# Kernel optimization log

Hardware: AMD Instinct MI355X
Metric: run time of the kernel (lower is better)

## Reference

```python
import jax, jax.numpy as jnp
from jax import lax
import numpy as np

B, C, H, W = 64, 1, 512, 512
N_MULT = 1  # len(mul_approx_func_arr)


def setup_inputs() -> dict:
    key = jax.random.key(0)
    k1, = jax.random.split(key, 1)
    # image-like pixel inputs in [0, 255)
    inp = jax.random.uniform(k1, (B, C, H, W), dtype=jnp.float32) * 255.0
    # Gaussian kernel params, tiled per multiplier variant (as in __init__)
    base = jnp.array([1.0, 2.0, 1.0, 2.0, 4.0, 2.0, 1.0, 2.0, 1.0], dtype=jnp.float32) / 16.0
    weight = jnp.tile(base[None, :], (N_MULT, 1))            # [N_MULT, 9]
    weight_factor = jnp.full((N_MULT, 1), 16.0, jnp.float32)  # [N_MULT, 1]
    return {"input": inp, "weight": weight, "weight_factor": weight_factor}


def _ste_quantize(x):
    # QuantizeGrad: forward = clamp(round(x), 0.001, inf); backward = identity (STE)
    q = jnp.clip(jnp.round(x), 0.001, None)
    return x + lax.stop_gradient(q - x)


def reference(input, weight, weight_factor):
    # in-place .data clamp (no grad through the clamp itself)
    wc_data = weight + lax.stop_gradient(jnp.clip(weight, 0.001, 0.999) - weight)
    wf_data = weight_factor + lax.stop_gradient(jnp.clip(weight_factor, 1.001, 254.999) - weight_factor)
    # hardtanh clamps (identity in-range after the data clamp)
    wc = jnp.clip(wc_data, 0.0, 1.0)
    wf = jnp.clip(wf_data, 1.0, 255.0)
    outs = []
    for ii in range(N_MULT):
        # weight_rounded: 9-element 3x3 kernel via STE quantization
        wr = _ste_quantize(wc[ii] * wf[ii])          # [9]
        kernel = wr.reshape(1, 1, 3, 3)
        # accurate_mult_only summed over the 9 taps == 3x3 conv, padding=1.
        # The approximate-multiplier forward value (mul_wrapper, emulated here as
        # exact multiply, index=1 accurate) is written into x.data, so forward
        # value and gradient path coincide under this emulation.
        y = lax.conv_general_dilated(
            input, kernel.astype(input.dtype),
            window_strides=(1, 1), padding=((1, 1), (1, 1)),
            dimension_numbers=("NCHW", "OIHW", "NCHW"))
        outs.append(y)
    # torch.stack(output, 0): [N_MULT, B, C, H, W]
    return jnp.stack(outs, 0)
```

## Files before the change

kernel.cpp:

```cpp
#include <hip/hip_runtime.h>


#define BB 64
#define HH 512
#define WW 512
#define W4 (WW / 4)
#define RR 4

__global__ __launch_bounds__(256) void gauss3x3_kernel(
    const float* __restrict__ in,
    const float* __restrict__ wgt,
    const float* __restrict__ wfac,
    float* __restrict__ out)
{
    float wf = fminf(fmaxf(wfac[0], 1.001f), 254.999f);
    float k[9];
#pragma unroll
    for (int i = 0; i < 9; ++i) {
        float wc = fminf(fmaxf(wgt[i], 0.001f), 0.999f);
        k[i] = fmaxf(rintf(wc * wf), 0.001f);
    }

    int tid   = blockIdx.x * blockDim.x + threadIdx.x;
    int x4    = tid & (W4 - 1);
    int strip = (tid >> 7) & (HH / RR - 1);
    int b     = tid >> 14;
    if (b >= BB) return;

    const int y0 = strip * RR;
    const int x0 = x4 * 4;
    const float* img  = in  + (size_t)b * HH * WW;
    float*       outp = out + (size_t)b * HH * WW;

    float4 acc[RR];
#pragma unroll
    for (int i = 0; i < RR; ++i) acc[i] = make_float4(0.f, 0.f, 0.f, 0.f);

#pragma unroll
    for (int j = 0; j < RR + 2; ++j) {
        const int ry = y0 - 1 + j;
        float4 c = make_float4(0.f, 0.f, 0.f, 0.f);
        float  l = 0.f, r = 0.f;
        if (ry >= 0 && ry < HH) {
            const float* row = img + (size_t)ry * WW;
            c = *(const float4*)(row + x0);
            l = (x0 > 0)      ? row[x0 - 1] : 0.f;
            r = (x0 + 4 < WW) ? row[x0 + 4] : 0.f;
        }
#pragma unroll
        for (int t = 0; t < 3; ++t) {
            const int i = j - t;
            if (i >= 0 && i < RR) {
                const float kl = k[t * 3 + 0];
                const float kc = k[t * 3 + 1];
                const float kr = k[t * 3 + 2];
                acc[i].x = fmaf(kl, l,   fmaf(kc, c.x, fmaf(kr, c.y, acc[i].x)));
                acc[i].y = fmaf(kl, c.x, fmaf(kc, c.y, fmaf(kr, c.z, acc[i].y)));
                acc[i].z = fmaf(kl, c.y, fmaf(kc, c.z, fmaf(kr, c.w, acc[i].z)));
                acc[i].w = fmaf(kl, c.z, fmaf(kc, c.w, fmaf(kr, r,   acc[i].w)));
            }
        }
    }

#pragma unroll
    for (int i = 0; i < RR; ++i)
        *(float4*)(outp + (size_t)(y0 + i) * WW + x0) = acc[i];
}

extern "C" void kernel_launch(void* const* d_in, const int* in_sizes, int n_in,
                              void* d_out, int out_size, void* d_ws, size_t ws_size,
                              hipStream_t stream) {
    const float* in   = (const float*)d_in[0];
    const float* wgt  = (const float*)d_in[1];
    const float* wfac = (const float*)d_in[2];
    float* out = (float*)d_out;

    const int total = BB * (HH / RR) * W4;
    const int block = 256;
    const int grid  = total / block;
    gauss3x3_kernel<<<grid, block, 0, stream>>>(in, wgt, wfac, out);
}
```

Baseline: 119.3 us.

## Map one wavefront per row strip and share halos via lane shuffles

Each 64-lane wavefront now covers a full 512-wide row strip, with every lane handling two float4 columns. Left and right halo pixels come from neighbouring lanes through shuffles instead of extra scalar global loads. Outputs are written with nontemporal stores to avoid cache pollution. The grid halves, so each thread does more work and holds more registers, and the shuffles add cross-lane instructions.

```diff
diff --git a/kernel.cpp b/kernel.cpp
--- a/kernel.cpp
+++ b/kernel.cpp
@@ -4,8 +4,9 @@
 #define BB 64
 #define HH 512
 #define WW 512
-#define W4 (WW / 4)
 #define RR 4
+
+typedef float vfloat4 __attribute__((ext_vector_type(4)));
 
 __global__ __launch_bounds__(256) void gauss3x3_kernel(
     const float* __restrict__ in,
@@ -21,31 +22,44 @@
         k[i] = fmaxf(rintf(wc * wf), 0.001f);
     }
 
-    int tid   = blockIdx.x * blockDim.x + threadIdx.x;
-    int x4    = tid & (W4 - 1);
-    int strip = (tid >> 7) & (HH / RR - 1);
-    int b     = tid >> 14;
+    const int gtid  = blockIdx.x * blockDim.x + threadIdx.x;
+    const int lane  = threadIdx.x & 63;
+    const int wid   = gtid >> 6;
+    const int strip = wid & (HH / RR - 1);
+    const int b     = wid >> 7;
     if (b >= BB) return;
 
     const int y0 = strip * RR;
-    const int x0 = x4 * 4;
     const float* img  = in  + (size_t)b * HH * WW;
     float*       outp = out + (size_t)b * HH * WW;
 
-    float4 acc[RR];
+    float4 acc1[RR], acc2[RR];
 #pragma unroll
-    for (int i = 0; i < RR; ++i) acc[i] = make_float4(0.f, 0.f, 0.f, 0.f);
+    for (int i = 0; i < RR; ++i) {
+        acc1[i] = make_float4(0.f, 0.f, 0.f, 0.f);
+        acc2[i] = make_float4(0.f, 0.f, 0.f, 0.f);
+    }
 
 #pragma unroll
     for (int j = 0; j < RR + 2; ++j) {
         const int ry = y0 - 1 + j;
-        float4 c = make_float4(0.f, 0.f, 0.f, 0.f);
-        float  l = 0.f, r = 0.f;
+        float4 c1 = make_float4(0.f, 0.f, 0.f, 0.f);
+        float4 c2 = c1;
+        float l1 = 0.f, r1 = 0.f, l2 = 0.f, r2 = 0.f;
         if (ry >= 0 && ry < HH) {
-            const float* row = img + (size_t)ry * WW;
-            c = *(const float4*)(row + x0);
-            l = (x0 > 0)      ? row[x0 - 1] : 0.f;
-            r = (x0 + 4 < WW) ? row[x0 + 4] : 0.f;
+            const float4* row4 = (const float4*)(img + (size_t)ry * WW);
+            c1 = row4[lane];
+            c2 = row4[lane + 64];
+            float l1n = __shfl_up(c1.w, 1);
+            float r1n = __shfl_down(c1.x, 1);
+            float l2n = __shfl_up(c2.w, 1);
+            float r2n = __shfl_down(c2.x, 1);
+            float b0  = __shfl(c2.x, 0);
+            float a63 = __shfl(c1.w, 63);
+            l1 = (lane == 0)  ? 0.f : l1n;
+            r1 = (lane == 63) ? b0  : r1n;
+            l2 = (lane == 0)  ? a63 : l2n;
+            r2 = (lane == 63) ? 0.f : r2n;
         }
 #pragma unroll
         for (int t = 0; t < 3; ++t) {
@@ -54,17 +68,26 @@
                 const float kl = k[t * 3 + 0];
                 const float kc = k[t * 3 + 1];
                 const float kr = k[t * 3 + 2];
-                acc[i].x = fmaf(kl, l,   fmaf(kc, c.x, fmaf(kr, c.y, acc[i].x)));
-                acc[i].y = fmaf(kl, c.x, fmaf(kc, c.y, fmaf(kr, c.z, acc[i].y)));
-                acc[i].z = fmaf(kl, c.y, fmaf(kc, c.z, fmaf(kr, c.w, acc[i].z)));
-                acc[i].w = fmaf(kl, c.z, fmaf(kc, c.w, fmaf(kr, r,   acc[i].w)));
+                acc1[i].x = fmaf(kl, l1,   fmaf(kc, c1.x, fmaf(kr, c1.y, acc1[i].x)));
+                acc1[i].y = fmaf(kl, c1.x, fmaf(kc, c1.y, fmaf(kr, c1.z, acc1[i].y)));
+                acc1[i].z = fmaf(kl, c1.y, fmaf(kc, c1.z, fmaf(kr, c1.w, acc1[i].z)));
+                acc1[i].w = fmaf(kl, c1.z, fmaf(kc, c1.w, fmaf(kr, r1,   acc1[i].w)));
+                acc2[i].x = fmaf(kl, l2,   fmaf(kc, c2.x, fmaf(kr, c2.y, acc2[i].x)));
+                acc2[i].y = fmaf(kl, c2.x, fmaf(kc, c2.y, fmaf(kr, c2.z, acc2[i].y)));
+                acc2[i].z = fmaf(kl, c2.y, fmaf(kc, c2.z, fmaf(kr, c2.w, acc2[i].z)));
+                acc2[i].w = fmaf(kl, c2.z, fmaf(kc, c2.w, fmaf(kr, r2,   acc2[i].w)));
             }
         }
     }
 
 #pragma unroll
-    for (int i = 0; i < RR; ++i)
-        *(float4*)(outp + (size_t)(y0 + i) * WW + x0) = acc[i];
+    for (int i = 0; i < RR; ++i) {
+        float* rowo = outp + (size_t)(y0 + i) * WW;
+        vfloat4 v1 = { acc1[i].x, acc1[i].y, acc1[i].z, acc1[i].w };
+        vfloat4 v2 = { acc2[i].x, acc2[i].y, acc2[i].z, acc2[i].w };
+        __builtin_nontemporal_store(v1, (vfloat4*)rowo + lane);
+        __builtin_nontemporal_store(v2, (vfloat4*)rowo + lane + 64);
+    }
 }
 
 extern "C" void kernel_launch(void* const* d_in, const int* in_sizes, int n_in,
@@ -75,7 +98,7 @@
     const float* wfac = (const float*)d_in[2];
     float* out = (float*)d_out;
 
-    const int total = BB * (HH / RR) * W4;
+    const int total = BB * (HH / RR) * 64;
     const int block = 256;
     const int grid  = total / block;
     gauss3x3_kernel<<<grid, block, 0, stream>>>(in, wgt, wfac, out);
```

Result: faster. 111.1 us (-6.9%).
